# Optimization experiments

Hardware: AMD Instinct MI355X
Metric: run time of the kernel (lower is better)

Reference implementation:

```python
import jax, jax.numpy as jnp
import numpy as np

B, S, E, H = 2, 2048, 1024, 16
D = E // H  # head_dim = 64


def setup_inputs() -> dict:
    key = jax.random.key(0)
    ks = jax.random.split(key, 12)
    sc = 1.0 / np.sqrt(E)
    inp = {
        "query": jax.random.normal(ks[0], (B, S, E), jnp.float32),
        "key": jax.random.normal(ks[1], (B, S, E), jnp.float32),
        "value": jax.random.normal(ks[2], (B, S, E), jnp.float32),
        # causal mask: 1 where attending is allowed, 0 where blocked
        "mask": jnp.tril(jnp.ones((S, S), jnp.int32))[None, None, :, :],
        "Wq": jax.random.normal(ks[3], (E, E), jnp.float32) * sc,
        "bq": jax.random.normal(ks[4], (E,), jnp.float32) * sc,
        "Wk": jax.random.normal(ks[5], (E, E), jnp.float32) * sc,
        "bk": jax.random.normal(ks[6], (E,), jnp.float32) * sc,
        "Wv": jax.random.normal(ks[7], (E, E), jnp.float32) * sc,
        "bv": jax.random.normal(ks[8], (E,), jnp.float32) * sc,
        "Wo": jax.random.normal(ks[9], (E, E), jnp.float32) * sc,
        "bo": jax.random.normal(ks[10], (E,), jnp.float32) * sc,
    }
    return inp


def reference(query, key, value, mask, Wq, bq, Wk, bk, Wv, bv, Wo, bo):
    scale = jnp.asarray(np.sqrt(D), query.dtype)
    # Linear projections (torch Linear: x @ W.T + b)
    Q = query @ Wq.T + bq
    K = key @ Wk.T + bk
    V = value @ Wv.T + bv
    # [B, S, E] -> [B, H, S, D]
    Q = Q.reshape(B, -1, H, D).transpose(0, 2, 1, 3)
    K = K.reshape(B, -1, H, D).transpose(0, 2, 1, 3)
    V = V.reshape(B, -1, H, D).transpose(0, 2, 1, 3)
    # full [B, H, Sq, Sk] score matrix, as in the source
    scores = jnp.einsum("bhqd,bhkd->bhqk", Q, K) / scale
    scores = jnp.where(mask == 0, jnp.asarray(-1e10, scores.dtype), scores)
    weights = jax.nn.softmax(scores, axis=-1)
    weighted = jnp.einsum("bhqk,bhkd->bhqd", weights, V)
    concat = weighted.transpose(0, 2, 1, 3).reshape(B, -1, E)
    return concat @ Wo.T + bo
```

## Files before the change

### kernel.cpp

```cpp
#include <hip/hip_runtime.h>
#include <math.h>

#define BB 2
#define SS 2048
#define EE 1024
#define HH 16
#define DD 64

typedef unsigned short u16;
typedef __attribute__((ext_vector_type(8))) short short8;
typedef __attribute__((ext_vector_type(4))) float f32x4;

__device__ __forceinline__ u16 f2bf(float x) {
    union { float f; unsigned u; } v; v.f = x;
    return (u16)((v.u + 0x7fffu + ((v.u >> 16) & 1u)) >> 16);
}

__device__ __forceinline__ float exp2_fast(float x) {
    float r;
    asm("v_exp_f32 %0, %1" : "=v"(r) : "v"(x));
    return r;
}

#define GLL16(gp, lp) \
    __builtin_amdgcn_global_load_lds( \
        (const __attribute__((address_space(1))) void*)(gp), \
        (__attribute__((address_space(3))) void*)(lp), 16, 0, 0)

#define QSCALE 0.18033688f

__global__ __launch_bounds__(256)
void cvt_bf16(const float* __restrict__ s0, const float* __restrict__ s1,
              const float* __restrict__ s2, const float* __restrict__ s3,
              u16* __restrict__ d0, u16* __restrict__ d1,
              u16* __restrict__ d2, u16* __restrict__ d3)
{
    const int z = blockIdx.y;
    const float* s; u16* d;
    switch (z) {
        case 0: s = s0; d = d0; break;
        case 1: s = s1; d = d1; break;
        case 2: s = s2; d = d2; break;
        default: s = s3; d = d3; break;
    }
    const int i = (blockIdx.x * 256 + threadIdx.x) * 8;
    float4 a = *(const float4*)(s + i);
    float4 b = *(const float4*)(s + i + 4);
    short8 r;
    r[0] = (short)f2bf(a.x); r[1] = (short)f2bf(a.y);
    r[2] = (short)f2bf(a.z); r[3] = (short)f2bf(a.w);
    r[4] = (short)f2bf(b.x); r[5] = (short)f2bf(b.y);
    r[6] = (short)f2bf(b.z); r[7] = (short)f2bf(b.w);
    *(short8*)(d + i) = r;
}

__global__ __launch_bounds__(256, 3)
void gemm_qkv(const float* __restrict__ Xq, const float* __restrict__ Xk,
              const float* __restrict__ Xv,
              const u16* __restrict__ Wqb, const u16* __restrict__ Wkb,
              const u16* __restrict__ Wvb,
              const float* __restrict__ bq, const float* __restrict__ bk,
              const float* __restrict__ bv,
              u16* __restrict__ Qh, u16* __restrict__ Kh, u16* __restrict__ Vth)
{
    __shared__ __align__(16) u16 LS[2][2][128][32];
#define LA (LS[0])
#define LB (LS[1])

    const int bid = blockIdx.x;
    const int swz = (bid & 7) * 96 + (bid >> 3);
    const int z   = swz >> 8;
    const int rem = swz & 255;
    const int m0  = (rem >> 3) * 128;
    const int n0  = (rem & 7) * 128;

    const float* X = (z == 0) ? Xq : (z == 1) ? Xk : Xv;
    const u16* Wt = (z == 0) ? Wqb : (z == 1) ? Wkb : Wvb;
    const float* bias = (z == 0) ? bq : (z == 1) ? bk : bv;
    u16* out = (z == 0) ? Qh : (z == 1) ? Kh : Vth;

    const int t = threadIdx.x;
    const int w = t >> 6, l = t & 63;
    const int ln = l & 15, hi = l >> 4;
    const int wr = w >> 1, wc = w & 1;

    const int ar = t >> 1, ah = t & 1;
    const float* Xrow = X + (size_t)(m0 + ar) * 1024 + ah * 16;
    const int fa   = (ar >> 1) & 3;
    const int gpa0 = (2 * ah)     ^ fa;
    const int gpa1 = (2 * ah + 1) ^ fa;

    const int brow = t >> 2, gp4 = t & 3;
    const int gl4  = gp4 ^ (brow & 3);
    const u16* Wp0 = Wt + (size_t)(n0 + brow) * 1024 + gl4 * 8;
    const u16* Wp1 = Wt + (size_t)(n0 + 64 + brow) * 1024 + gl4 * 8;

    f32x4 acc[4][4];
    #pragma unroll
    for (int i = 0; i < 4; i++)
        #pragma unroll
        for (int j = 0; j < 4; j++)
            acc[i][j] = (f32x4){0.f, 0.f, 0.f, 0.f};

    float4 a0, a1, a2, a3;

#define ISSUE(buf, k0_) {                                                    \
        GLL16(Wp0 + (k0_), &LB[buf][brow][gp4 * 8]);                         \
        GLL16(Wp1 + (k0_), &LB[buf][brow + 64][gp4 * 8]);                    \
        a0 = *(const float4*)(Xrow + (k0_));                                 \
        a1 = *(const float4*)(Xrow + (k0_) + 4);                             \
        a2 = *(const float4*)(Xrow + (k0_) + 8);                             \
        a3 = *(const float4*)(Xrow + (k0_) + 12);                            \
    }

#define CVTWRITE(buf) {                                                      \
        uint4 u0, u1;                                                        \
        u0.x = f2bf(a0.x) | ((unsigned)f2bf(a0.y) << 16);                    \
        u0.y = f2bf(a0.z) | ((unsigned)f2bf(a0.w) << 16);                    \
        u0.z = f2bf(a1.x) | ((unsigned)f2bf(a1.y) << 16);                    \
        u0.w = f2bf(a1.z) | ((unsigned)f2bf(a1.w) << 16);                    \
        u1.x = f2bf(a2.x) | ((unsigned)f2bf(a2.y) << 16);                    \
        u1.y = f2bf(a2.z) | ((unsigned)f2bf(a2.w) << 16);                    \
        u1.z = f2bf(a3.x) | ((unsigned)f2bf(a3.y) << 16);                    \
        u1.w = f2bf(a3.z) | ((unsigned)f2bf(a3.w) << 16);                    \
        *(uint4*)&LA[buf][ar][gpa0 * 8] = u0;                                \
        *(uint4*)&LA[buf][ar][gpa1 * 8] = u1;                                \
    }

    ISSUE(0, 0);
    CVTWRITE(0);
    __syncthreads();

    short8 af[4], bf[4];
    int cur = 0;
    for (int it = 0; it < 32; ++it) {
        const int k0 = it * 32;
        if (it < 31) ISSUE(cur ^ 1, k0 + 32);
        #pragma unroll
        for (int mi = 0; mi < 4; mi++)
            af[mi] = *(const short8*)&LA[cur][wr*64 + mi*16 + ln][(hi ^ ((ln >> 1) & 3)) * 8];
        #pragma unroll
        for (int nj = 0; nj < 4; nj++)
            bf[nj] = *(const short8*)&LB[cur][wc*64 + nj*16 + ln][(hi ^ (ln & 3)) * 8];
        #pragma unroll
        for (int mi = 0; mi < 4; mi++)
            #pragma unroll
            for (int nj = 0; nj < 4; nj++)
                acc[mi][nj] = __builtin_amdgcn_mfma_f32_16x16x32_bf16(
                    af[mi], bf[nj], acc[mi][nj], 0, 0, 0);
        if (it < 31) CVTWRITE(cur ^ 1);
        __syncthreads();
        cur ^= 1;
    }
#undef ISSUE
#undef CVTWRITE

    if (z == 2) {
        u16* T = &LS[0][0][0][0];
        #pragma unroll
        for (int mi = 0; mi < 4; mi++) {
            #pragma unroll
            for (int nj = 0; nj < 4; nj++) {
                const int nc = wc * 64 + nj * 16 + ln;
                const float bv2 = bias[n0 + nc];
                const int sr0 = wr * 64 + mi * 16 + hi * 4;
                uint2 pk;
                pk.x = f2bf(acc[mi][nj][0] + bv2)
                     | ((unsigned)f2bf(acc[mi][nj][1] + bv2) << 16);
                pk.y = f2bf(acc[mi][nj][2] + bv2)
                     | ((unsigned)f2bf(acc[mi][nj][3] + bv2) << 16);
                const int gp = (sr0 >> 2) ^ (nc & 31);
                *(uint2*)&T[nc * 128 + gp * 4] = pk;
            }
        }
        __syncthreads();
        const int b  = m0 >> 11, s0 = m0 & 2047;
        const int sidx = t & 15;
        const int ncr0 = t >> 4;
        #pragma unroll
        for (int i = 0; i < 8; i++) {
            const int nc = ncr0 + i * 16;
            const int a  = sidx * 2;
            const int pa = a ^ (nc & 31);
            const int pb = (a + 1) ^ (nc & 31);
            uint2 lo  = *(const uint2*)&T[nc * 128 + pa * 4];
            uint2 hi2 = *(const uint2*)&T[nc * 128 + pb * 4];
            uint4 vd = make_uint4(lo.x, lo.y, hi2.x, hi2.y);
            const int h = (n0 >> 6) + (nc >> 6);
            const int d = nc & 63;
            *(uint4*)&out[(((size_t)(b * HH + h) * 64 + d) << 11) + s0 + sidx * 8] = vd;
        }
    } else {
        #pragma unroll
        for (int mi = 0; mi < 4; mi++) {
            #pragma unroll
            for (int nj = 0; nj < 4; nj++) {
                const int nb = n0 + wc * 64 + nj * 16 + ln;
                const float bv2 = bias[nb];
                const int h = nb >> 6, d = nb & 63;
                #pragma unroll
                for (int r = 0; r < 4; r++) {
                    const int m = m0 + wr * 64 + mi * 16 + hi * 4 + r;
                    float v = acc[mi][nj][r] + bv2;
                    if (z == 0) v *= QSCALE;
                    const int b = m >> 11, s = m & 2047;
                    out[((((size_t)(b * HH + h)) << 11) + s) * 64 + d] = f2bf(v);
                }
            }
        }
    }
#undef LA
#undef LB
}

__global__ __launch_bounds__(256)
void gemm_out(const u16* __restrict__ Xb, const u16* __restrict__ Wb,
              const float* __restrict__ bias, float* __restrict__ outp)
{
    __shared__ __align__(16) u16 As[2][64][32];
    __shared__ __align__(16) u16 Bs[2][128][32];

    const int bid = blockIdx.x;
    const int swz = (bid & 7) * 64 + (bid >> 3);
    const int m0  = (swz >> 3) * 64;
    const int n0  = (swz & 7) * 128;

    const int t = threadIdx.x;
    const int w = t >> 6, l = t & 63;
    const int ln = l & 15, hi = l >> 4;
    const int wr = w >> 1, wc = w & 1;

    const int row0 = t >> 2, gp4 = t & 3;
    const int gl4  = gp4 ^ (row0 & 3);

    f32x4 acc[2][4];
    #pragma unroll
    for (int i = 0; i < 2; i++)
        #pragma unroll
        for (int j = 0; j < 4; j++)
            acc[i][j] = (f32x4){0.f, 0.f, 0.f, 0.f};

#define OSTAGE(buf, k0_) { \
    GLL16(Xb + (size_t)(m0 + row0) * 1024 + (k0_) + gl4 * 8,        \
          &As[buf][row0][gp4 * 8]);                                  \
    GLL16(Wb + (size_t)(n0 + row0) * 1024 + (k0_) + gl4 * 8,        \
          &Bs[buf][row0][gp4 * 8]);                                  \
    GLL16(Wb + (size_t)(n0 + 64 + row0) * 1024 + (k0_) + gl4 * 8,   \
          &Bs[buf][row0 + 64][gp4 * 8]); }

    OSTAGE(0, 0);
    __syncthreads();
    int cur = 0;
    for (int k0 = 0; k0 < 1024; k0 += 32) {
        if (k0 + 32 < 1024) OSTAGE(cur ^ 1, k0 + 32);
        short8 af[2], bfr[4];
        #pragma unroll
        for (int mi = 0; mi < 2; mi++)
            af[mi] = *(const short8*)&As[cur][wr*32 + mi*16 + ln][(hi ^ (ln & 3))*8];
        #pragma unroll
        for (int nj = 0; nj < 4; nj++)
            bfr[nj] = *(const short8*)&Bs[cur][wc*64 + nj*16 + ln][(hi ^ (ln & 3))*8];
        #pragma unroll
        for (int mi = 0; mi < 2; mi++)
            #pragma unroll
            for (int nj = 0; nj < 4; nj++)
                acc[mi][nj] = __builtin_amdgcn_mfma_f32_16x16x32_bf16(
                    af[mi], bfr[nj], acc[mi][nj], 0, 0, 0);
        __syncthreads();
        cur ^= 1;
    }
#undef OSTAGE

    #pragma unroll
    for (int mi = 0; mi < 2; mi++) {
        #pragma unroll
        for (int nj = 0; nj < 4; nj++) {
            const int nb = n0 + wc * 64 + nj * 16 + ln;
            const float bv2 = bias[nb];
            #pragma unroll
            for (int r = 0; r < 4; r++) {
                const int m = m0 + wr * 32 + mi * 16 + hi * 4 + r;
                outp[(size_t)m * 1024 + nb] = acc[mi][nj][r] + bv2;
            }
        }
    }
}

__global__ __launch_bounds__(256)
void attn_mfma(const u16* __restrict__ Qh, const u16* __restrict__ Kh,
               const u16* __restrict__ Vt, u16* __restrict__ Cc)
{
    __shared__ __align__(16) u16 Ks[2][2][4][64][8];
    __shared__ __align__(16) u16 Vs[2][2][4][64][8];
    __shared__ __align__(16) u16 Ps[4][16][64];
    const int bh = blockIdx.x;
    const int y  = 31 - blockIdx.y;
    const int q0 = y * 64;
    const int t = threadIdx.x, w = t >> 6, l = t & 63;
    const int ln = l & 15, hi = l >> 4;
    const size_t base = (size_t)bh * SS * DD;
    const int qg = q0 + w * 16 + ln;

    short8 qf0, qf1;
    {
        const u16* qp = Qh + base + (size_t)qg * 64 + hi * 8;
        qf0 = *(const short8*)qp;
        qf1 = *(const short8*)(qp + 32);
    }
    f32x4 o[4];
    #pragma unroll
    for (int dj = 0; dj < 4; dj++) o[dj] = (f32x4){0.f, 0.f, 0.f, 0.f};
    float mrun = -INFINITY, lrun = 0.f;

#define STAGE(buf, key0_)                                                        \
    {                                                                            \
        _Pragma("unroll")                                                        \
        for (int i_ = 0; i_ < 4; i_++) {                                         \
            const int id_ = w + i_ * 4;                                          \
            if (id_ < 8) {                                                       \
                const int dc_ = id_ >> 2, kg_ = id_ & 3;                         \
                const u16* gp_ = Kh + base + (size_t)((key0_) + l) * 64          \
                                 + dc_ * 32 + kg_ * 8;                           \
                GLL16(gp_, &Ks[buf][dc_][kg_][0][0]);                            \
            } else {                                                             \
                const int kc_ = (id_ >> 2) & 1, kg_ = id_ & 3;                   \
                const u16* gp_ = Vt + base + (size_t)l * SS + (key0_)            \
                                 + kc_ * 32 + kg_ * 8;                           \
                GLL16(gp_, &Vs[buf][kc_][kg_][0][0]);                            \
            }                                                                    \
        }                                                                        \
    }

    STAGE(0, 0);
    __syncthreads();
    int cur = 0;
    const int nkt = y + 1;
    for (int kt = 0; kt < nkt; kt++) {
        const int key0 = kt * 64;
        if (kt + 1 < nkt) STAGE(cur ^ 1, key0 + 64);

        f32x4 st[4];
        #pragma unroll
        for (int kt4 = 0; kt4 < 4; kt4++) {
            short8 ka = *(const short8*)&Ks[cur][0][hi][kt4 * 16 + ln][0];
            short8 kb = *(const short8*)&Ks[cur][1][hi][kt4 * 16 + ln][0];
            f32x4 zz = (f32x4){0.f, 0.f, 0.f, 0.f};
            zz = __builtin_amdgcn_mfma_f32_16x16x32_bf16(ka, qf0, zz, 0, 0, 0);
            zz = __builtin_amdgcn_mfma_f32_16x16x32_bf16(kb, qf1, zz, 0, 0, 0);
            st[kt4] = zz;
        }
        if (kt == y) {
            #pragma unroll
            for (int kt4 = 0; kt4 < 4; kt4++)
                #pragma unroll
                for (int r = 0; r < 4; r++)
                    if (key0 + kt4 * 16 + hi * 4 + r > qg)
                        st[kt4][r] = -INFINITY;
        }

        float tmax = -INFINITY;
        #pragma unroll
        for (int kt4 = 0; kt4 < 4; kt4++)
            #pragma unroll
            for (int r = 0; r < 4; r++)
                tmax = fmaxf(tmax, st[kt4][r]);
        tmax = fmaxf(tmax, __shfl_xor(tmax, 16));
        tmax = fmaxf(tmax, __shfl_xor(tmax, 32));
        if (__ballot(tmax > mrun + 8.f)) {
            const float mnew = fmaxf(mrun, tmax);
            const float alpha = exp2_fast(mrun - mnew);
            lrun *= alpha;
            mrun = mnew;
            #pragma unroll
            for (int r = 0; r < 4; r++) {
                const float ar = __shfl(alpha, hi * 4 + r);
                #pragma unroll
                for (int dj = 0; dj < 4; dj++) o[dj][r] *= ar;
            }
        }
        float p[4][4];
        float lsum = 0.f;
        #pragma unroll
        for (int kt4 = 0; kt4 < 4; kt4++)
            #pragma unroll
            for (int r = 0; r < 4; r++) {
                p[kt4][r] = exp2_fast(st[kt4][r] - mrun);
                lsum += p[kt4][r];
            }
        lsum += __shfl_xor(lsum, 16);
        lsum += __shfl_xor(lsum, 32);
        lrun += lsum;

        char* prow = ((char*)Ps) + (w * 16 + ln) * 128 + (hi & 1) * 8;
        #pragma unroll
        for (int kt4 = 0; kt4 < 4; kt4++) {
            unsigned dw0, dw1;
            asm("v_cvt_pk_bf16_f32 %0, %1, %2" : "=v"(dw0)
                : "v"(p[kt4][0]), "v"(p[kt4][1]));
            asm("v_cvt_pk_bf16_f32 %0, %1, %2" : "=v"(dw1)
                : "v"(p[kt4][2]), "v"(p[kt4][3]));
            const int g = (2 * kt4 + (hi >> 1)) ^ (ln & 7);
            *(uint2*)(prow + g * 16) = make_uint2(dw0, dw1);
        }

        #pragma unroll
        for (int kc = 0; kc < 2; kc++) {
            const int gr = (kc * 4 + hi) ^ (ln & 7);
            short8 pa = *(const short8*)(((char*)Ps) + (w * 16 + ln) * 128 + gr * 16);
            #pragma unroll
            for (int dj = 0; dj < 4; dj++) {
                short8 vb = *(const short8*)&Vs[cur][kc][hi][dj * 16 + ln][0];
                o[dj] = __builtin_amdgcn_mfma_f32_16x16x32_bf16(pa, vb, o[dj], 0, 0, 0);
            }
        }
        __syncthreads();
        cur ^= 1;
    }
#undef STAGE

    const float inv = 1.f / lrun;
    #pragma unroll
    for (int r = 0; r < 4; r++) {
        const float ir = __shfl(inv, hi * 4 + r);
        const int s = q0 + w * 16 + hi * 4 + r;
        const size_t ob = ((size_t)(bh >> 4) * SS + s) * EE + (bh & 15) * 64;
        #pragma unroll
        for (int dj = 0; dj < 4; dj++)
            Cc[ob + dj * 16 + ln] = f2bf(o[dj][r] * ir);
    }
}

extern "C" void kernel_launch(void* const* d_in, const int* in_sizes, int n_in,
                              void* d_out, int out_size, void* d_ws, size_t ws_size,
                              hipStream_t stream)
{
    (void)in_sizes; (void)n_in; (void)out_size; (void)ws_size;
    const float* query = (const float*)d_in[0];
    const float* key   = (const float*)d_in[1];
    const float* value = (const float*)d_in[2];
    const float* Wq = (const float*)d_in[4];
    const float* bq = (const float*)d_in[5];
    const float* Wk = (const float*)d_in[6];
    const float* bk = (const float*)d_in[7];
    const float* Wv = (const float*)d_in[8];
    const float* bv = (const float*)d_in[9];
    const float* Wo = (const float*)d_in[10];
    const float* bo = (const float*)d_in[11];
    float* out = (float*)d_out;

    char* ws = (char*)d_ws;
    u16* Wqb = (u16*)(ws + 25165824);
    u16* Wkb = (u16*)(ws + 27262976);
    u16* Wvb = (u16*)(ws + 29360128);
    u16* Wob = (u16*)(ws + 31457280);
    u16* Qh  = (u16*)(ws + 33554432);
    u16* Kh  = (u16*)(ws + 41943040);
    u16* Vth = (u16*)(ws + 50331648);
    u16* Cc  = (u16*)(ws + 58720256);

    cvt_bf16<<<dim3(512, 4), 256, 0, stream>>>(
        Wq, Wk, Wv, Wo, Wqb, Wkb, Wvb, Wob);

    gemm_qkv<<<768, 256, 0, stream>>>(
        query, key, value, Wqb, Wkb, Wvb, bq, bk, bv, Qh, Kh, Vth);
    attn_mfma<<<dim3(32, 32), 256, 0, stream>>>(Qh, Kh, Vth, Cc);
    gemm_out<<<512, 256, 0, stream>>>(Cc, Wob, bo, out);
}
```

Before: 118.7 us.

## Deepen QKV projection GEMM pipeline with manual waitcnts and set MFMA priority in attention

The fused QKV projection GEMM's main loop is unrolled by two with fixed LDS buffers. A-operand fp32 loads are issued two k-steps ahead into alternating register sets, and __syncthreads is replaced by explicit vmcnt/lgkmcnt waits, raw s_barrier and sched_barrier fences. This aims to hide global load latency behind the MFMA work. The attention kernel wraps its MFMA blocks in s_setprio to favour matrix issue across waves. The cost is more live registers and hand-counted waitcnt values that must match the number of loads in flight.

```diff
diff --git a/kernel.cpp b/kernel.cpp
--- a/kernel.cpp
+++ b/kernel.cpp
@@ -26,6 +26,14 @@
     __builtin_amdgcn_global_load_lds( \
         (const __attribute__((address_space(1))) void*)(gp), \
         (__attribute__((address_space(3))) void*)(lp), 16, 0, 0)
+
+#define BARRIER do { asm volatile("" ::: "memory"); \
+                     __builtin_amdgcn_s_barrier();  \
+                     asm volatile("" ::: "memory"); } while (0)
+#define VMW4 asm volatile("s_waitcnt vmcnt(4)" ::: "memory")
+#define VMW0 asm volatile("s_waitcnt vmcnt(0)" ::: "memory")
+#define LG0  asm volatile("s_waitcnt lgkmcnt(0)" ::: "memory")
+#define SCHED0 __builtin_amdgcn_sched_barrier(0)
 
 #define QSCALE 0.18033688f
 
@@ -102,61 +110,88 @@
         for (int j = 0; j < 4; j++)
             acc[i][j] = (f32x4){0.f, 0.f, 0.f, 0.f};
 
-    float4 a0, a1, a2, a3;
-
-#define ISSUE(buf, k0_) {                                                    \
+    float4 e0, e1, e2, e3;
+    float4 o0, o1, o2, o3;
+
+#define ISSUE_B(buf, k0_) {                                                  \
         GLL16(Wp0 + (k0_), &LB[buf][brow][gp4 * 8]);                         \
         GLL16(Wp1 + (k0_), &LB[buf][brow + 64][gp4 * 8]);                    \
-        a0 = *(const float4*)(Xrow + (k0_));                                 \
-        a1 = *(const float4*)(Xrow + (k0_) + 4);                             \
-        a2 = *(const float4*)(Xrow + (k0_) + 8);                             \
-        a3 = *(const float4*)(Xrow + (k0_) + 12);                            \
-    }
-
-#define CVTWRITE(buf) {                                                      \
+    }
+#define LOAD_A(S0, S1, S2, S3, k0_) {                                        \
+        S0 = *(const float4*)(Xrow + (k0_));                                 \
+        S1 = *(const float4*)(Xrow + (k0_) + 4);                             \
+        S2 = *(const float4*)(Xrow + (k0_) + 8);                             \
+        S3 = *(const float4*)(Xrow + (k0_) + 12);                            \
+    }
+#define CVT_A(buf, S0, S1, S2, S3) {                                         \
         uint4 u0, u1;                                                        \
-        u0.x = f2bf(a0.x) | ((unsigned)f2bf(a0.y) << 16);                    \
-        u0.y = f2bf(a0.z) | ((unsigned)f2bf(a0.w) << 16);                    \
-        u0.z = f2bf(a1.x) | ((unsigned)f2bf(a1.y) << 16);                    \
-        u0.w = f2bf(a1.z) | ((unsigned)f2bf(a1.w) << 16);                    \
-        u1.x = f2bf(a2.x) | ((unsigned)f2bf(a2.y) << 16);                    \
-        u1.y = f2bf(a2.z) | ((unsigned)f2bf(a2.w) << 16);                    \
-        u1.z = f2bf(a3.x) | ((unsigned)f2bf(a3.y) << 16);                    \
-        u1.w = f2bf(a3.z) | ((unsigned)f2bf(a3.w) << 16);                    \
+        u0.x = f2bf(S0.x) | ((unsigned)f2bf(S0.y) << 16);                    \
+        u0.y = f2bf(S0.z) | ((unsigned)f2bf(S0.w) << 16);                    \
+        u0.z = f2bf(S1.x) | ((unsigned)f2bf(S1.y) << 16);                    \
+        u0.w = f2bf(S1.z) | ((unsigned)f2bf(S1.w) << 16);                    \
+        u1.x = f2bf(S2.x) | ((unsigned)f2bf(S2.y) << 16);                    \
+        u1.y = f2bf(S2.z) | ((unsigned)f2bf(S2.w) << 16);                    \
+        u1.z = f2bf(S3.x) | ((unsigned)f2bf(S3.y) << 16);                    \
+        u1.w = f2bf(S3.z) | ((unsigned)f2bf(S3.w) << 16);                    \
         *(uint4*)&LA[buf][ar][gpa0 * 8] = u0;                                \
         *(uint4*)&LA[buf][ar][gpa1 * 8] = u1;                                \
     }
-
-    ISSUE(0, 0);
-    CVTWRITE(0);
-    __syncthreads();
+#define COMPUTE(la_, lb_) {                                                  \
+        _Pragma("unroll")                                                    \
+        for (int mi = 0; mi < 4; mi++)                                       \
+            af[mi] = *(const short8*)&LA[la_][wr*64 + mi*16 + ln]            \
+                         [(hi ^ ((ln >> 1) & 3)) * 8];                       \
+        _Pragma("unroll")                                                    \
+        for (int nj = 0; nj < 4; nj++)                                       \
+            bf[nj] = *(const short8*)&LB[lb_][wc*64 + nj*16 + ln]            \
+                         [(hi ^ (ln & 3)) * 8];                              \
+        _Pragma("unroll")                                                    \
+        for (int mi = 0; mi < 4; mi++)                                       \
+            _Pragma("unroll")                                                \
+            for (int nj = 0; nj < 4; nj++)                                   \
+                acc[mi][nj] = __builtin_amdgcn_mfma_f32_16x16x32_bf16(       \
+                    af[mi], bf[nj], acc[mi][nj], 0, 0, 0);                   \
+    }
 
     short8 af[4], bf[4];
-    int cur = 0;
-    for (int it = 0; it < 32; ++it) {
-        const int k0 = it * 32;
-        if (it < 31) ISSUE(cur ^ 1, k0 + 32);
-        #pragma unroll
-        for (int mi = 0; mi < 4; mi++)
-            af[mi] = *(const short8*)&LA[cur][wr*64 + mi*16 + ln][(hi ^ ((ln >> 1) & 3)) * 8];
-        #pragma unroll
-        for (int nj = 0; nj < 4; nj++)
-            bf[nj] = *(const short8*)&LB[cur][wc*64 + nj*16 + ln][(hi ^ (ln & 3)) * 8];
-        #pragma unroll
-        for (int mi = 0; mi < 4; mi++)
-            #pragma unroll
-            for (int nj = 0; nj < 4; nj++)
-                acc[mi][nj] = __builtin_amdgcn_mfma_f32_16x16x32_bf16(
-                    af[mi], bf[nj], acc[mi][nj], 0, 0, 0);
-        if (it < 31) CVTWRITE(cur ^ 1);
-        __syncthreads();
-        cur ^= 1;
-    }
-#undef ISSUE
-#undef CVTWRITE
+
+    LOAD_A(e0, e1, e2, e3, 0);
+    CVT_A(0, e0, e1, e2, e3);
+    ISSUE_B(0, 0); SCHED0;
+    LOAD_A(o0, o1, o2, o3, 32); SCHED0;
+    VMW4;
+    LG0; BARRIER;
+
+    for (int it = 0; it < 15; ++it) {
+        const int k0 = it * 64;
+        ISSUE_B(1, k0 + 32); SCHED0;
+        LOAD_A(e0, e1, e2, e3, k0 + 64); SCHED0;
+        COMPUTE(0, 0);
+        CVT_A(1, o0, o1, o2, o3);
+        VMW4;
+        LG0; BARRIER;
+        ISSUE_B(0, k0 + 64); SCHED0;
+        LOAD_A(o0, o1, o2, o3, k0 + 96); SCHED0;
+        COMPUTE(1, 1);
+        CVT_A(0, e0, e1, e2, e3);
+        VMW4;
+        LG0; BARRIER;
+    }
+    ISSUE_B(1, 992); SCHED0;
+    COMPUTE(0, 0);
+    CVT_A(1, o0, o1, o2, o3);
+    VMW0;
+    LG0; BARRIER;
+    COMPUTE(1, 1);
+#undef ISSUE_B
+#undef LOAD_A
+#undef CVT_A
+#undef COMPUTE
+
+    u16* T = &LS[0][0][0][0];
+    const int b = m0 >> 11;
 
     if (z == 2) {
-        u16* T = &LS[0][0][0][0];
         #pragma unroll
         for (int mi = 0; mi < 4; mi++) {
             #pragma unroll
@@ -174,7 +209,7 @@
             }
         }
         __syncthreads();
-        const int b  = m0 >> 11, s0 = m0 & 2047;
+        const int s0 = m0 & 2047;
         const int sidx = t & 15;
         const int ncr0 = t >> 4;
         #pragma unroll
@@ -203,7 +238,7 @@
                     const int m = m0 + wr * 64 + mi * 16 + hi * 4 + r;
                     float v = acc[mi][nj][r] + bv2;
                     if (z == 0) v *= QSCALE;
-                    const int b = m >> 11, s = m & 2047;
+                    const int s = m & 2047;
                     out[((((size_t)(b * HH + h)) << 11) + s) * 64 + d] = f2bf(v);
                 }
             }
@@ -340,6 +375,7 @@
         if (kt + 1 < nkt) STAGE(cur ^ 1, key0 + 64);
 
         f32x4 st[4];
+        __builtin_amdgcn_s_setprio(1);
         #pragma unroll
         for (int kt4 = 0; kt4 < 4; kt4++) {
             short8 ka = *(const short8*)&Ks[cur][0][hi][kt4 * 16 + ln][0];
@@ -349,6 +385,7 @@
             zz = __builtin_amdgcn_mfma_f32_16x16x32_bf16(kb, qf1, zz, 0, 0, 0);
             st[kt4] = zz;
         }
+        __builtin_amdgcn_s_setprio(0);
         if (kt == y) {
             #pragma unroll
             for (int kt4 = 0; kt4 < 4; kt4++)
@@ -403,6 +440,7 @@
             *(uint2*)(prow + g * 16) = make_uint2(dw0, dw1);
         }
 
+        __builtin_amdgcn_s_setprio(1);
         #pragma unroll
         for (int kc = 0; kc < 2; kc++) {
             const int gr = (kc * 4 + hi) ^ (ln & 7);
@@ -413,6 +451,7 @@
                 o[dj] = __builtin_amdgcn_mfma_f32_16x16x32_bf16(pa, vb, o[dj], 0, 0, 0);
             }
         }
+        __builtin_amdgcn_s_setprio(0);
         __syncthreads();
         cur ^= 1;
     }
```

Result: no change. 117.5 us (median of 3 runs) (-1.0%).
